# Kernel tuning notes

Hardware: AMD Instinct MI355X
Metric: run time of the kernel (lower is better)

## Reference

```python
import jax, jax.numpy as jnp
import numpy as np

GAMMA = 1.0  # rbf kernel bandwidth (config.gamma)
LN_EPS = 1e-5


def _layernorm(x, w):
    # LayerNorm(d_embed, bias=False): normalize last dim, scale by w
    mu = jnp.mean(x, axis=-1, keepdims=True)
    var = jnp.var(x, axis=-1, keepdims=True)
    return (x - mu) * jax.lax.rsqrt(var + LN_EPS) * w


def setup_inputs() -> dict:
    key = jax.random.key(0)
    ks = jax.random.split(key, 8)
    B, S, D, H = 4, 1024, 256, 8
    x = jax.random.normal(ks[0], (B, S, D), dtype=jnp.float32)
    e = jax.random.normal(ks[1], (B, S, D), dtype=jnp.float32)
    p = jax.random.normal(ks[2], (B, S, D), dtype=jnp.float32)
    W_q = 0.02 * jax.random.normal(ks[3], (H, D, D), dtype=jnp.float32)
    W_k = 0.02 * jax.random.normal(ks[4], (H, D, D), dtype=jnp.float32)
    W_v = 0.02 * jax.random.normal(ks[5], (H, D, D), dtype=jnp.float32)
    n_layer = 12
    W_o = (0.02 / np.sqrt(2 * n_layer)) * jax.random.normal(ks[6], (H * D, D), dtype=jnp.float32)
    ln_w = jnp.ones((D,), dtype=jnp.float32)
    return {"x": x, "e": e, "p": p, "W_q": W_q, "W_k": W_k, "W_v": W_v, "W_o": W_o, "ln_w": ln_w}


def reference(x, e, p, W_q, W_k, W_v, W_o, ln_w):
    # use_ppe=False path: only x is used (e, p ignored)
    B, S, D = x.shape
    H = W_q.shape[0]
    xn = _layernorm(x, ln_w)                                   # [B,S,D]
    # per-head full-size projections: Q/K/V [B,H,S,D]
    Q = jnp.einsum('bsd,hde->bhse', xn, W_q)
    K = jnp.einsum('bsd,hde->bhse', xn, W_k)
    V = jnp.einsum('bsd,hde->bhse', xn, W_v)
    # rbf kernel: exp(-gamma * ||q-k||^2) via the expansion trick
    q2 = jnp.sum(Q * Q, axis=-1)                               # [B,H,S]
    k2 = jnp.sum(K * K, axis=-1)                               # [B,H,S]
    qk = jnp.einsum('bhse,bhte->bhst', Q, K)                   # [B,H,S,S]
    dist2 = jnp.maximum(q2[..., :, None] + k2[..., None, :] - 2.0 * qk, 0.0)
    attn = jnp.exp(-GAMMA * dist2)                             # [B,H,S,S]
    # nto=True -> no causal mask; dropout=0 (eval) -> identity
    out = jnp.einsum('bhst,bhte->bhse', attn, V)               # [B,H,S,D]
    out = jnp.swapaxes(out, 1, 2).reshape(B, S, H * D)         # concat heads
    return out @ W_o                                           # [B,S,D]
```

## Files before the change

kernel.cpp:

```cpp
#include <hip/hip_runtime.h>
#include <cstdint>
#include <cstddef>

#define B_ 4
#define S_ 1024
#define D_ 256
#define H_ 8

typedef unsigned short u16;
typedef __attribute__((ext_vector_type(8))) short short8v;
typedef __attribute__((ext_vector_type(8))) _Float16 half8v;
typedef __attribute__((ext_vector_type(4))) float f32x4;
typedef __attribute__((ext_vector_type(4))) u16 u16x4;
typedef __attribute__((ext_vector_type(8))) u16 u16x8;

__device__ inline u16 f2b(float f) {
  unsigned u = __builtin_bit_cast(unsigned, f);
  unsigned r = (u + 0x7FFFu + ((u >> 16) & 1u)) >> 16;
  return (u16)r;
}
__device__ inline float b2f(u16 h) {
  return __builtin_bit_cast(float, ((unsigned)h) << 16);
}
__device__ inline u16 f2h(float f) {
  return __builtin_bit_cast(u16, (_Float16)f);
}
__device__ inline f32x4 mfma16(short8v a, short8v b, f32x4 c) {
  return __builtin_amdgcn_mfma_f32_16x16x32_bf16(a, b, c, 0, 0, 0);
}
__device__ inline f32x4 mfma16h(half8v a, half8v b, f32x4 c) {
  return __builtin_amdgcn_mfma_f32_16x16x32_f16(a, b, c, 0, 0, 0);
}
__device__ __forceinline__ void gl16(const u16* g, u16* l) {
  __builtin_amdgcn_global_load_lds((const uint32_t*)g, (uint32_t*)l, 16, 0, 0);
}

__global__ __launch_bounds__(256) void lnwt_kernel(
    const float* __restrict__ x, const float* __restrict__ w,
    const float* __restrict__ Wq, const float* __restrict__ Wk,
    const float* __restrict__ Wv, const float* __restrict__ Wo,
    u16* __restrict__ xf, u16* __restrict__ WTf, u16* __restrict__ WoTf) {
  const int bid = blockIdx.x;
  const int tid = threadIdx.x;
  if (bid < 4096) {
    const int row = bid;
    const float v = x[(size_t)row * D_ + tid];
    float s = v, s2 = v * v;
#pragma unroll
    for (int off = 32; off > 0; off >>= 1) {
      s  += __shfl_down(s, off);
      s2 += __shfl_down(s2, off);
    }
    __shared__ float rs[4], rs2[4];
    __shared__ float smu, srr;
    const int wid = tid >> 6, lane = tid & 63;
    if (lane == 0) { rs[wid] = s; rs2[wid] = s2; }
    __syncthreads();
    if (tid == 0) {
      const float a = rs[0] + rs[1] + rs[2] + rs[3];
      const float b = rs2[0] + rs2[1] + rs2[2] + rs2[3];
      const float mu  = a * (1.0f / D_);
      const float var = b * (1.0f / D_) - mu * mu;
      smu = mu; srr = rsqrtf(var + 1e-5f);
    }
    __syncthreads();
    const float r = (v - smu) * srr * w[tid];
    xf[(size_t)row * D_ + tid] = f2h(r);
  } else {
    __shared__ float t[32][33];
    const int z = bid - 4096;
    const int tc = tid & 31, tr = tid >> 5;
    if (z < 1536) {
      const int wm = z >> 6;
      const int mat = wm >> 3, h = wm & 7;
      const float* src = (mat == 0 ? Wq : mat == 1 ? Wk : Wv) + (size_t)h * 65536;
      const int t6 = z & 63;
      const int r0 = (t6 >> 3) * 32, c0 = (t6 & 7) * 32;
      u16* df = WTf + (size_t)wm * 65536;
#pragma unroll
      for (int i = 0; i < 4; ++i)
        t[tr + i * 8][tc] = src[(size_t)(r0 + tr + i * 8) * 256 + c0 + tc];
      __syncthreads();
#pragma unroll
      for (int i = 0; i < 4; ++i) {
        const float v = t[tc][tr + i * 8];
        df[(size_t)(c0 + tr + i * 8) * 256 + r0 + tc] = f2h(v);
      }
    } else {
      const int z2 = z - 1536;
      const int r0 = (z2 >> 3) * 32, c0 = (z2 & 7) * 32;
#pragma unroll
      for (int i = 0; i < 4; ++i)
        t[tr + i * 8][tc] = Wo[(size_t)(r0 + tr + i * 8) * 256 + c0 + tc];
      __syncthreads();
#pragma unroll
      for (int i = 0; i < 4; ++i) {
        const float v = t[tc][tr + i * 8];
        WoTf[(size_t)(c0 + tr + i * 8) * 2048 + r0 + tc] = f2b(v);
      }
    }
  }
}

__global__ __launch_bounds__(256, 3) void proj_kernel(
    const u16* __restrict__ xf, const u16* __restrict__ WTf,
    u16* __restrict__ Qf, u16* __restrict__ Kf,
    u16* __restrict__ Vt, float* __restrict__ k2g) {
  const int z = blockIdx.y;
  const int mat = z >> 3, h = z & 7;
  const int xb = blockIdx.x;

  const u16 *Ap, *Bp;
  int arow0, brow0;
  if (mat < 2) {
    Ap = WTf + (size_t)z * 65536; arow0 = (xb >> 5) * 128;
    Bp = xf;                      brow0 = (xb & 31) * 128;
  } else {
    Ap = xf;                      arow0 = (xb & 31) * 128;
    Bp = WTf + (size_t)z * 65536; brow0 = (xb >> 5) * 128;
  }

  __shared__ u16 LS[2 * 128 * 64];
  u16* AS = LS; u16* BS = LS + 128 * 64;
  char* LSb = (char*)LS;
  char* ASb = (char*)AS; char* BSb = (char*)BS;

  const int tid = threadIdx.x;
  const int w = tid >> 6, lane = tid & 63;
  const int lr = lane & 15, lh = lane >> 4;
  const int wm = w >> 1, wn = w & 1;

  f32x4 acc[4][4];
#pragma unroll
  for (int i = 0; i < 4; ++i)
#pragma unroll
    for (int j = 0; j < 4; ++j) acc[i][j] = (f32x4){0.f, 0.f, 0.f, 0.f};

  for (int k0 = 0; k0 < 256; k0 += 64) {
    __syncthreads();
#pragma unroll
    for (int j = 0; j < 4; ++j) {
      const int c0 = j * 256 + w * 64;
      const int c = c0 + lane;
      const int m = c >> 3, sl = c & 7;
      const int l = sl ^ (m & 7);
      gl16(Ap + (size_t)(arow0 + m) * 256 + k0 + l * 8, AS + c0 * 8);
    }
#pragma unroll
    for (int j = 0; j < 4; ++j) {
      const int c0 = j * 256 + w * 64;
      const int c = c0 + lane;
      const int n = c >> 3, sl = c & 7;
      const int l = sl ^ (n & 7);
      gl16(Bp + (size_t)(brow0 + n) * 256 + k0 + l * 8, BS + c0 * 8);
    }
    __syncthreads();

#pragma unroll
    for (int ks = 0; ks < 2; ++ks) {
      half8v af[4], bf[4];
#pragma unroll
      for (int mf = 0; mf < 4; ++mf) {
        const int m = wm * 64 + mf * 16 + lr;
        af[mf] = *reinterpret_cast<const half8v*>(
            ASb + m * 128 + (((ks * 4 + lh) * 16) ^ ((m & 7) << 4)));
      }
#pragma unroll
      for (int nf = 0; nf < 4; ++nf) {
        const int n = wn * 64 + nf * 16 + lr;
        bf[nf] = *reinterpret_cast<const half8v*>(
            BSb + n * 128 + (((ks * 4 + lh) * 16) ^ ((n & 7) << 4)));
      }
      __builtin_amdgcn_s_setprio(1);
#pragma unroll
      for (int mf = 0; mf < 4; ++mf)
#pragma unroll
        for (int nf = 0; nf < 4; ++nf)
          acc[mf][nf] = mfma16h(af[mf], bf[nf], acc[mf][nf]);
      __builtin_amdgcn_s_setprio(0);
    }
  }

  __syncthreads();

  if (mat < 2) {
    u16* Hf = (mat == 0) ? Qf : Kf;
#pragma unroll
    for (int mf = 0; mf < 4; ++mf)
#pragma unroll
      for (int nf = 0; nf < 4; ++nf) {
        const int sl_ = wn * 64 + nf * 16 + lr;
        const int el_ = wm * 64 + mf * 16 + lh * 4;
        u16x4 hv;
#pragma unroll
        for (int r = 0; r < 4; ++r) hv[r] = f2h(acc[mf][nf][r]);
        *reinterpret_cast<u16x4*>(LSb + sl_ * 256 + ((el_ * 2) ^ ((sl_ & 7) << 4))) = hv;
      }
    if (mat == 1) {
#pragma unroll
      for (int nf = 0; nf < 4; ++nf) {
        float p = 0.f;
#pragma unroll
        for (int mf = 0; mf < 4; ++mf)
#pragma unroll
          for (int r = 0; r < 4; ++r) {
            const float v = (float)(_Float16)acc[mf][nf][r];
            p = fmaf(v, v, p);
          }
        p += __shfl_xor(p, 16);
        p += __shfl_xor(p, 32);
        if (lh == 0) {
          const int s = brow0 + wn * 64 + nf * 16 + lr;
          const int bb = s >> 10;
          atomicAdd(&k2g[(size_t)(bb * H_ + h) * S_ + (s & 1023)], p);
        }
      }
    }
    __syncthreads();
#pragma unroll
    for (int i = 0; i < 8; ++i) {
      const int c = i * 256 + tid;
      const int sl_ = c >> 4, ch = c & 15;
      const u16x8 v = *reinterpret_cast<const u16x8*>(
          LSb + sl_ * 256 + ((ch * 16) ^ ((sl_ & 7) << 4)));
      const int s = brow0 + sl_;
      const int bb = s >> 10;
      *reinterpret_cast<u16x8*>(
          Hf + ((size_t)(bb * H_ + h) * S_ + (s & 1023)) * D_ + arow0 + ch * 8) = v;
    }
  } else {
#pragma unroll
    for (int mf = 0; mf < 4; ++mf)
#pragma unroll
      for (int nf = 0; nf < 4; ++nf) {
        const int dl_ = wn * 64 + nf * 16 + lr;
        const int sl_ = wm * 64 + mf * 16 + lh * 4;
        u16x4 hv;
#pragma unroll
        for (int r = 0; r < 4; ++r) hv[r] = f2b(acc[mf][nf][r]);
        *reinterpret_cast<u16x4*>(LSb + dl_ * 256 + ((sl_ * 2) ^ ((dl_ & 7) << 4))) = hv;
      }
    __syncthreads();
#pragma unroll
    for (int i = 0; i < 8; ++i) {
      const int c = i * 256 + tid;
      const int dl_ = c >> 4, ch = c & 15;
      const u16x8 v = *reinterpret_cast<const u16x8*>(
          LSb + dl_ * 256 + ((ch * 16) ^ ((dl_ & 7) << 4)));
      const int d = brow0 + dl_;
      const int sg = arow0 + ch * 8;
      const int bb = sg >> 10;
      *reinterpret_cast<u16x8*>(
          Vt + ((size_t)(bb * H_ + h) * D_ + d) * S_ + (sg & 1023)) = v;
    }
  }
}

__global__ __launch_bounds__(256, 2) void attn_kernel(
    const u16* __restrict__ Qf, const u16* __restrict__ Kf,
    const u16* __restrict__ Vt, const float* __restrict__ k2,
    u16* __restrict__ aOf) {
  const int bh  = blockIdx.x;
  const int qt  = blockIdx.y;
  const int tid = threadIdx.x;
  const int w = tid >> 6, lane = tid & 63;
  const int lr = lane & 15, lh = lane >> 4;
  const int qg = w >> 1, kvh = w & 1;

  __shared__ u16 KS[64 * 256];
  __shared__ u16 VS[256 * 64];
  __shared__ u16 PS[64 * 64];
  __shared__ float q2s[64];
  char* KB = (char*)KS; char* VB = (char*)VS; char* PB = (char*)PS;

  half8v qf[2][8];
#pragma unroll
  for (int at = 0; at < 2; ++at) {
    const int qrow = qt * 64 + qg * 32 + at * 16 + lr;
    const size_t qbase = ((size_t)(bh * S_) + qrow) * D_ + lh * 8;
#pragma unroll
    for (int ds = 0; ds < 8; ++ds)
      qf[at][ds] = *reinterpret_cast<const half8v*>(Qf + qbase + ds * 32);
  }
#pragma unroll
  for (int at = 0; at < 2; ++at) {
    float p = 0.f;
#pragma unroll
    for (int ds = 0; ds < 8; ++ds)
#pragma unroll
      for (int j = 0; j < 8; ++j) {
        const float v = (float)qf[at][ds][j];
        p = fmaf(v, v, p);
      }
    p += __shfl_xor(p, 16);
    p += __shfl_xor(p, 32);
    if (kvh == 0 && lh == 0) q2s[qg * 32 + at * 16 + lr] = p;
  }
  __syncthreads();
  float q2v[2][4];
#pragma unroll
  for (int at = 0; at < 2; ++at)
#pragma unroll
    for (int r = 0; r < 4; ++r)
      q2v[at][r] = q2s[qg * 32 + at * 16 + lh * 4 + r];

  f32x4 oacc[4][4];
#pragma unroll
  for (int i = 0; i < 4; ++i)
#pragma unroll
    for (int j = 0; j < 4; ++j) oacc[i][j] = (f32x4){0.f, 0.f, 0.f, 0.f};

  const size_t kgbase = (size_t)(bh * S_);
  const size_t vgbase = (size_t)(bh * D_);

  for (int kt = 0; kt < 16; ++kt) {
    __syncthreads();
#pragma unroll
    for (int j = 0; j < 8; ++j) {
      const int c0 = j * 256 + w * 64;
      const int c = c0 + lane;
      const int row = c >> 5, slot = c & 31;
      gl16(Kf + (kgbase + kt * 64 + row) * D_ + ((slot ^ (row & 7)) << 3), KS + c0 * 8);
    }
    __syncthreads();
#pragma unroll
    for (int j = 0; j < 8; ++j) {
      const int c0 = j * 256 + w * 64;
      const int c = c0 + lane;
      const int d = c >> 3, slot = c & 7;
      gl16(Vt + (vgbase + d) * S_ + kt * 64 + ((slot ^ (d & 7)) << 3), VS + c0 * 8);
    }

    f32x4 pacc[2][2];
#pragma unroll
    for (int at = 0; at < 2; ++at)
#pragma unroll
      for (int bt = 0; bt < 2; ++bt) pacc[at][bt] = (f32x4){0.f, 0.f, 0.f, 0.f};
#pragma unroll
    for (int ds = 0; ds < 8; ++ds) {
      half8v kf[2];
#pragma unroll
      for (int bt = 0; bt < 2; ++bt) {
        const int krow = kvh * 32 + bt * 16 + lr;
        kf[bt] = *reinterpret_cast<const half8v*>(
            KB + krow * 512 + (((ds * 64) + lh * 16) ^ ((krow & 7) << 4)));
      }
      __builtin_amdgcn_s_setprio(1);
#pragma unroll
      for (int at = 0; at < 2; ++at)
#pragma unroll
        for (int bt = 0; bt < 2; ++bt)
          pacc[at][bt] = mfma16h(qf[at][ds], kf[bt], pacc[at][bt]);
      __builtin_amdgcn_s_setprio(0);
    }
#pragma unroll
    for (int bt = 0; bt < 2; ++bt) {
      const int kv = kvh * 32 + bt * 16 + lr;
      const float k2v = k2[bh * S_ + kt * 64 + kv];
#pragma unroll
      for (int at = 0; at < 2; ++at)
#pragma unroll
        for (int r = 0; r < 4; ++r) {
          float d2 = q2v[at][r] + k2v - 2.0f * pacc[at][bt][r];
          d2 = fmaxf(d2, 0.f);
          const int q = qg * 32 + at * 16 + lh * 4 + r;
          *reinterpret_cast<u16*>(PB + q * 128 + ((kv * 2) ^ ((q & 7) << 4))) =
              f2b(__expf(-d2));
        }
    }
    __syncthreads();

    short8v vfr[4][2];
#pragma unroll
    for (int dt = 0; dt < 4; ++dt)
#pragma unroll
      for (int ks = 0; ks < 2; ++ks) {
        const int d = w * 64 + dt * 16 + lr;
        vfr[dt][ks] = *reinterpret_cast<const short8v*>(
            VB + d * 128 + (((ks * 64) + lh * 16) ^ ((d & 7) << 4)));
      }
#pragma unroll
    for (int pq = 0; pq < 4; ++pq) {
      short8v pa[2];
#pragma unroll
      for (int ks = 0; ks < 2; ++ks) {
        const int q = pq * 16 + lr;
        pa[ks] = *reinterpret_cast<const short8v*>(
            PB + q * 128 + (((ks * 64) + lh * 16) ^ ((q & 7) << 4)));
      }
      __builtin_amdgcn_s_setprio(1);
#pragma unroll
      for (int dt = 0; dt < 4; ++dt) {
        oacc[pq][dt] = mfma16(pa[0], vfr[dt][0], oacc[pq][dt]);
        oacc[pq][dt] = mfma16(pa[1], vfr[dt][1], oacc[pq][dt]);
      }
      __builtin_amdgcn_s_setprio(0);
    }
  }

  const int bb = bh >> 3, hh = bh & 7;
#pragma unroll
  for (int pq = 0; pq < 4; ++pq)
#pragma unroll
    for (int dt = 0; dt < 4; ++dt)
#pragma unroll
      for (int r = 0; r < 4; ++r) {
        const int s = qt * 64 + pq * 16 + lh * 4 + r;
        const int d = w * 64 + dt * 16 + lr;
        const size_t idx = ((size_t)(bb * S_) + s) * (H_ * D_) + hh * D_ + d;
        aOf[idx] = f2b(oacc[pq][dt][r]);
      }
}

__global__ __launch_bounds__(512, 4) void outproj_kernel(
    const u16* __restrict__ WoTf, const u16* __restrict__ aOf,
    u16* __restrict__ pbuf) {
  const int xb = blockIdx.x;
  const int kc = blockIdx.y;
  const int bm = xb >> 5, bn = xb & 31;
  const int arow0 = bm * 128, brow0 = bn * 128;

  __shared__ u16 AhS[128 * 64], BhS[128 * 64];
  char* AhB = (char*)AhS; char* BhB = (char*)BhS;

  const int tid = threadIdx.x;
  const int w = tid >> 6, lane = tid & 63;
  const int lr = lane & 15, lh = lane >> 4;
  const int wr = w >> 2, wc = w & 3;

  f32x4 acc[4][2];
#pragma unroll
  for (int i = 0; i < 4; ++i)
#pragma unroll
    for (int j = 0; j < 2; ++j) acc[i][j] = (f32x4){0.f, 0.f, 0.f, 0.f};

  for (int k0 = kc * 512; k0 < kc * 512 + 512; k0 += 64) {
#pragma unroll
    for (int i = 0; i < 2; ++i) {
      const int c = tid + i * 512;
      const int row = c >> 3, slot = c & 7;
      const int off = row * 128 + ((slot * 16) ^ ((row & 7) << 4));
      const size_t ga = (size_t)(arow0 + row) * 2048 + k0 + slot * 8;
      const size_t gb = (size_t)(brow0 + row) * 2048 + k0 + slot * 8;
      *reinterpret_cast<short8v*>(AhB + off) = *reinterpret_cast<const short8v*>(WoTf + ga);
      *reinterpret_cast<short8v*>(BhB + off) = *reinterpret_cast<const short8v*>(aOf + gb);
    }
    __syncthreads();
#pragma unroll
    for (int ks = 0; ks < 2; ++ks) {
      short8v afh[4], bfh[2];
#pragma unroll
      for (int mf = 0; mf < 4; ++mf) {
        const int m = wr * 64 + mf * 16 + lr;
        afh[mf] = *reinterpret_cast<const short8v*>(
            AhB + m * 128 + (((ks * 64) + lh * 16) ^ ((m & 7) << 4)));
      }
#pragma unroll
      for (int nf = 0; nf < 2; ++nf) {
        const int n = wc * 32 + nf * 16 + lr;
        bfh[nf] = *reinterpret_cast<const short8v*>(
            BhB + n * 128 + (((ks * 64) + lh * 16) ^ ((n & 7) << 4)));
      }
      __builtin_amdgcn_s_setprio(1);
#pragma unroll
      for (int mf = 0; mf < 4; ++mf)
#pragma unroll
        for (int nf = 0; nf < 2; ++nf)
          acc[mf][nf] = mfma16(afh[mf], bfh[nf], acc[mf][nf]);
      __builtin_amdgcn_s_setprio(0);
    }
    __syncthreads();
  }

  u16* pout = pbuf + (size_t)kc * (4096 * 256);
#pragma unroll
  for (int mf = 0; mf < 4; ++mf) {
    const int e0 = bm * 128 + wr * 64 + mf * 16 + lh * 4;
#pragma unroll
    for (int nf = 0; nf < 2; ++nf) {
      const int s = bn * 128 + wc * 32 + nf * 16 + lr;
      u16x4 hv;
#pragma unroll
      for (int r = 0; r < 4; ++r) hv[r] = f2b(acc[mf][nf][r]);
      *reinterpret_cast<u16x4*>(pout + (size_t)s * D_ + e0) = hv;
    }
  }
}

__global__ __launch_bounds__(256) void reduce_kernel(const u16* __restrict__ pbuf,
                                                     float* __restrict__ out) {
  const size_t i = ((size_t)blockIdx.x * 256 + threadIdx.x) * 8;
  const size_t C = (size_t)4096 * 256;
  const u16x8 a = *reinterpret_cast<const u16x8*>(pbuf + i);
  const u16x8 b = *reinterpret_cast<const u16x8*>(pbuf + C + i);
  const u16x8 c = *reinterpret_cast<const u16x8*>(pbuf + 2 * C + i);
  const u16x8 d = *reinterpret_cast<const u16x8*>(pbuf + 3 * C + i);
  float4 o0, o1;
  float* o = &o0.x;
#pragma unroll
  for (int j = 0; j < 8; ++j) {
    const float v = b2f((u16)a[j]) + b2f((u16)b[j]) + b2f((u16)c[j]) + b2f((u16)d[j]);
    if (j < 4) (&o0.x)[j] = v; else (&o1.x)[j - 4] = v;
  }
  (void)o;
  *reinterpret_cast<float4*>(out + i)     = o0;
  *reinterpret_cast<float4*>(out + i + 4) = o1;
}

extern "C" void kernel_launch(void* const* d_in, const int* in_sizes, int n_in,
                              void* d_out, int out_size, void* d_ws, size_t ws_size,
                              hipStream_t stream) {
  (void)in_sizes; (void)n_in; (void)out_size; (void)ws_size;
  const float* x   = (const float*)d_in[0];
  const float* Wq  = (const float*)d_in[3];
  const float* Wk  = (const float*)d_in[4];
  const float* Wv  = (const float*)d_in[5];
  const float* Wo  = (const float*)d_in[6];
  const float* lnw = (const float*)d_in[7];
  float* out = (float*)d_out;

  char* ws = (char*)d_ws;
  u16*  xf   = (u16*)(ws);
  u16*  WTf  = (u16*)(ws + ((size_t)2   << 20));
  u16*  WoTf = (u16*)(ws + ((size_t)5   << 20));
  float* k2  = (float*)(ws + ((size_t)6  << 20));
  u16*  Qf   = (u16*)(ws + ((size_t)8   << 20));
  u16*  Kf   = (u16*)(ws + ((size_t)24  << 20));
  u16*  Vt   = (u16*)(ws + ((size_t)40  << 20));
  u16*  aOf  = (u16*)(ws + ((size_t)56  << 20));
  u16*  pbuf = (u16*)(ws + ((size_t)72  << 20));

  hipMemsetAsync(k2, 0, (size_t)B_ * H_ * S_ * sizeof(float), stream);
  lnwt_kernel<<<dim3(6144), dim3(256), 0, stream>>>(x, lnw, Wq, Wk, Wv, Wo, xf, WTf, WoTf);
  proj_kernel<<<dim3(64, 24), dim3(256), 0, stream>>>(xf, WTf, Qf, Kf, Vt, k2);
  attn_kernel<<<dim3(32, 16), dim3(256), 0, stream>>>(Qf, Kf, Vt, k2, aOf);
  outproj_kernel<<<dim3(64, 4), dim3(512), 0, stream>>>(WoTf, aOf, pbuf);
  reduce_kernel<<<dim3(512), dim3(256), 0, stream>>>(pbuf, out);
}
```

Before: 98.53 us.

## Prefetch next K/V tile during compute and drop q2 shared-memory exchange

Restructures the attention kernel's main loop so the next K tile is loaded right after QK^T finishes and the next V tile right after PV finishes, using explicit vmcnt waits and raw barriers instead of __syncthreads. The QK MFMA operands are swapped so each lane keeps its own q2 row in a register, which removes the shared-memory q2 buffer and one barrier, and lets P be written as packed 4-element stores with vectorised k2 loads. The goal is to hide global-to-LDS latency behind MFMA work and cut synchronisation and scattered LDS writes. The hand-written waitcnt counts and the wraparound prefetch on the last iteration rely on exact ordering of outstanding loads, so any miscount would cause a race.

```diff
diff --git a/kernel.cpp b/kernel.cpp
--- a/kernel.cpp
+++ b/kernel.cpp
@@ -270,7 +270,6 @@
   __shared__ u16 KS[64 * 256];
   __shared__ u16 VS[256 * 64];
   __shared__ u16 PS[64 * 64];
-  __shared__ float q2s[64];
   char* KB = (char*)KS; char* VB = (char*)VS; char* PB = (char*)PS;
 
   half8v qf[2][8];
@@ -282,6 +281,26 @@
     for (int ds = 0; ds < 8; ++ds)
       qf[at][ds] = *reinterpret_cast<const half8v*>(Qf + qbase + ds * 32);
   }
+
+  const size_t kgbase = (size_t)(bh * S_);
+  const size_t vgbase = (size_t)(bh * D_);
+
+#pragma unroll
+  for (int j = 0; j < 8; ++j) {
+    const int c0 = j * 256 + w * 64;
+    const int c = c0 + lane;
+    const int row = c >> 5, slot = c & 31;
+    gl16(Kf + (kgbase + row) * D_ + ((slot ^ (row & 7)) << 3), KS + c0 * 8);
+  }
+#pragma unroll
+  for (int j = 0; j < 8; ++j) {
+    const int c0 = j * 256 + w * 64;
+    const int c = c0 + lane;
+    const int d = c >> 3, slot = c & 7;
+    gl16(Vt + (vgbase + d) * S_ + ((slot ^ (d & 7)) << 3), VS + c0 * 8);
+  }
+
+  float q2v[2];
 #pragma unroll
   for (int at = 0; at < 2; ++at) {
     float p = 0.f;
@@ -294,15 +313,12 @@
       }
     p += __shfl_xor(p, 16);
     p += __shfl_xor(p, 32);
-    if (kvh == 0 && lh == 0) q2s[qg * 32 + at * 16 + lr] = p;
-  }
-  __syncthreads();
-  float q2v[2][4];
-#pragma unroll
-  for (int at = 0; at < 2; ++at)
-#pragma unroll
-    for (int r = 0; r < 4; ++r)
-      q2v[at][r] = q2s[qg * 32 + at * 16 + lh * 4 + r];
+    q2v[at] = p;
+  }
+
+  asm volatile("s_waitcnt vmcnt(8)" ::: "memory");
+  __builtin_amdgcn_sched_barrier(0);
+  __builtin_amdgcn_s_barrier();
 
   f32x4 oacc[4][4];
 #pragma unroll
@@ -310,93 +326,109 @@
 #pragma unroll
     for (int j = 0; j < 4; ++j) oacc[i][j] = (f32x4){0.f, 0.f, 0.f, 0.f};
 
-  const size_t kgbase = (size_t)(bh * S_);
-  const size_t vgbase = (size_t)(bh * D_);
-
   for (int kt = 0; kt < 16; ++kt) {
-    __syncthreads();
+    const int ktn = (kt + 1) & 15;
+
+    f32x4 k2v[2];
+#pragma unroll
+    for (int bt = 0; bt < 2; ++bt)
+      k2v[bt] = *reinterpret_cast<const f32x4*>(
+          k2 + (size_t)bh * S_ + kt * 64 + kvh * 32 + bt * 16 + lh * 4);
+
+    f32x4 pacc[2][2];
+#pragma unroll
+    for (int at = 0; at < 2; ++at)
+#pragma unroll
+      for (int bt = 0; bt < 2; ++bt) pacc[at][bt] = (f32x4){0.f, 0.f, 0.f, 0.f};
+#pragma unroll
+    for (int ds = 0; ds < 8; ++ds) {
+      half8v kf[2];
+#pragma unroll
+      for (int bt = 0; bt < 2; ++bt) {
+        const int krow = kvh * 32 + bt * 16 + lr;
+        kf[bt] = *reinterpret_cast<const half8v*>(
+            KB + krow * 512 + (((ds * 64) + lh * 16) ^ ((krow & 7) << 4)));
+      }
+      __builtin_amdgcn_s_setprio(1);
+#pragma unroll
+      for (int at = 0; at < 2; ++at)
+#pragma unroll
+        for (int bt = 0; bt < 2; ++bt)
+          pacc[at][bt] = mfma16h(kf[bt], qf[at][ds], pacc[at][bt]);
+      __builtin_amdgcn_s_setprio(0);
+    }
+    asm volatile("s_waitcnt lgkmcnt(0)" ::: "memory");
+    __builtin_amdgcn_sched_barrier(0);
+    __builtin_amdgcn_s_barrier();
+
 #pragma unroll
     for (int j = 0; j < 8; ++j) {
       const int c0 = j * 256 + w * 64;
       const int c = c0 + lane;
       const int row = c >> 5, slot = c & 31;
-      gl16(Kf + (kgbase + kt * 64 + row) * D_ + ((slot ^ (row & 7)) << 3), KS + c0 * 8);
-    }
-    __syncthreads();
+      gl16(Kf + (kgbase + ktn * 64 + row) * D_ + ((slot ^ (row & 7)) << 3), KS + c0 * 8);
+    }
+
+#pragma unroll
+    for (int at = 0; at < 2; ++at) {
+      const int q = qg * 32 + at * 16 + lr;
+#pragma unroll
+      for (int bt = 0; bt < 2; ++bt) {
+        const int kv0 = kvh * 32 + bt * 16 + lh * 4;
+        u16x4 pv;
+#pragma unroll
+        for (int r = 0; r < 4; ++r) {
+          float d2 = q2v[at] + k2v[bt][r] - 2.0f * pacc[at][bt][r];
+          d2 = fmaxf(d2, 0.f);
+          pv[r] = f2b(__expf(-d2));
+        }
+        *reinterpret_cast<u16x4*>(PB + q * 128 + ((kv0 * 2) ^ ((q & 7) << 4))) = pv;
+      }
+    }
+    asm volatile("s_waitcnt vmcnt(8) lgkmcnt(0)" ::: "memory");
+    __builtin_amdgcn_sched_barrier(0);
+    __builtin_amdgcn_s_barrier();
+
+    short8v vfr[4][2];
+#pragma unroll
+    for (int dt = 0; dt < 4; ++dt)
+#pragma unroll
+      for (int ks = 0; ks < 2; ++ks) {
+        const int d = w * 64 + dt * 16 + lr;
+        vfr[dt][ks] = *reinterpret_cast<const short8v*>(
+            VB + d * 128 + (((ks * 64) + lh * 16) ^ ((d & 7) << 4)));
+      }
+#pragma unroll
+    for (int pq = 0; pq < 4; ++pq) {
+      short8v pa[2];
+#pragma unroll
+      for (int ks = 0; ks < 2; ++ks) {
+        const int q = pq * 16 + lr;
+        pa[ks] = *reinterpret_cast<const short8v*>(
+            PB + q * 128 + (((ks * 64) + lh * 16) ^ ((q & 7) << 4)));
+      }
+      __builtin_amdgcn_s_setprio(1);
+#pragma unroll
+      for (int dt = 0; dt < 4; ++dt) {
+        oacc[pq][dt] = mfma16(pa[0], vfr[dt][0], oacc[pq][dt]);
+        oacc[pq][dt] = mfma16(pa[1], vfr[dt][1], oacc[pq][dt]);
+      }
+      __builtin_amdgcn_s_setprio(0);
+    }
+    asm volatile("s_waitcnt vmcnt(0) lgkmcnt(0)" ::: "memory");
+    __builtin_amdgcn_sched_barrier(0);
+    __builtin_amdgcn_s_barrier();
+
 #pragma unroll
     for (int j = 0; j < 8; ++j) {
       const int c0 = j * 256 + w * 64;
       const int c = c0 + lane;
       const int d = c >> 3, slot = c & 7;
-      gl16(Vt + (vgbase + d) * S_ + kt * 64 + ((slot ^ (d & 7)) << 3), VS + c0 * 8);
-    }
-
-    f32x4 pacc[2][2];
-#pragma unroll
-    for (int at = 0; at < 2; ++at)
-#pragma unroll
-      for (int bt = 0; bt < 2; ++bt) pacc[at][bt] = (f32x4){0.f, 0.f, 0.f, 0.f};
-#pragma unroll
-    for (int ds = 0; ds < 8; ++ds) {
-      half8v kf[2];
-#pragma unroll
-      for (int bt = 0; bt < 2; ++bt) {
-        const int krow = kvh * 32 + bt * 16 + lr;
-        kf[bt] = *reinterpret_cast<const half8v*>(
-            KB + krow * 512 + (((ds * 64) + lh * 16) ^ ((krow & 7) << 4)));
-      }
-      __builtin_amdgcn_s_setprio(1);
-#pragma unroll
-      for (int at = 0; at < 2; ++at)
-#pragma unroll
-        for (int bt = 0; bt < 2; ++bt)
-          pacc[at][bt] = mfma16h(qf[at][ds], kf[bt], pacc[at][bt]);
-      __builtin_amdgcn_s_setprio(0);
-    }
-#pragma unroll
-    for (int bt = 0; bt < 2; ++bt) {
-      const int kv = kvh * 32 + bt * 16 + lr;
-      const float k2v = k2[bh * S_ + kt * 64 + kv];
-#pragma unroll
-      for (int at = 0; at < 2; ++at)
-#pragma unroll
-        for (int r = 0; r < 4; ++r) {
-          float d2 = q2v[at][r] + k2v - 2.0f * pacc[at][bt][r];
-          d2 = fmaxf(d2, 0.f);
-          const int q = qg * 32 + at * 16 + lh * 4 + r;
-          *reinterpret_cast<u16*>(PB + q * 128 + ((kv * 2) ^ ((q & 7) << 4))) =
-              f2b(__expf(-d2));
-        }
-    }
-    __syncthreads();
-
-    short8v vfr[4][2];
-#pragma unroll
-    for (int dt = 0; dt < 4; ++dt)
-#pragma unroll
-      for (int ks = 0; ks < 2; ++ks) {
-        const int d = w * 64 + dt * 16 + lr;
-        vfr[dt][ks] = *reinterpret_cast<const short8v*>(
-            VB + d * 128 + (((ks * 64) + lh * 16) ^ ((d & 7) << 4)));
-      }
-#pragma unroll
-    for (int pq = 0; pq < 4; ++pq) {
-      short8v pa[2];
-#pragma unroll
-      for (int ks = 0; ks < 2; ++ks) {
-        const int q = pq * 16 + lr;
-        pa[ks] = *reinterpret_cast<const short8v*>(
-            PB + q * 128 + (((ks * 64) + lh * 16) ^ ((q & 7) << 4)));
-      }
-      __builtin_amdgcn_s_setprio(1);
-#pragma unroll
-      for (int dt = 0; dt < 4; ++dt) {
-        oacc[pq][dt] = mfma16(pa[0], vfr[dt][0], oacc[pq][dt]);
-        oacc[pq][dt] = mfma16(pa[1], vfr[dt][1], oacc[pq][dt]);
-      }
-      __builtin_amdgcn_s_setprio(0);
-    }
-  }
+      gl16(Vt + (vgbase + d) * S_ + ktn * 64 + ((slot ^ (d & 7)) << 3), VS + c0 * 8);
+    }
+  }
+
+  asm volatile("s_waitcnt vmcnt(0)" ::: "memory");
 
   const int bb = bh >> 3, hh = bh & 7;
 #pragma unroll
```

New measurement: 97.74 us. About the same (-0.8%).

## Load K/V fragments directly from global into registers, double-buffer P tile

Applied to the files above, without the earlier changes.

The attention kernel stops staging K and V tiles through shared memory. Each wave loads its K and V MFMA fragments straight from global memory into registers, and the QK MFMA is transposed (K as the A operand) so that q2 and k2 can be taken per lane without a shared-memory exchange. The P tile is double-buffered so only one barrier per iteration remains, which cuts LDS traffic, LDS footprint and synchronisation. The cost is redundant global/L2 reads, since both wave pairs and all q-tiles reload the same K/V, plus higher register pressure.

```diff
diff --git a/kernel.cpp b/kernel.cpp
--- a/kernel.cpp
+++ b/kernel.cpp
@@ -267,11 +267,8 @@
   const int lr = lane & 15, lh = lane >> 4;
   const int qg = w >> 1, kvh = w & 1;
 
-  __shared__ u16 KS[64 * 256];
-  __shared__ u16 VS[256 * 64];
-  __shared__ u16 PS[64 * 64];
-  __shared__ float q2s[64];
-  char* KB = (char*)KS; char* VB = (char*)VS; char* PB = (char*)PS;
+  __shared__ u16 PS[2][64 * 64];
+  char* PB = (char*)PS;
 
   half8v qf[2][8];
 #pragma unroll
@@ -282,6 +279,8 @@
     for (int ds = 0; ds < 8; ++ds)
       qf[at][ds] = *reinterpret_cast<const half8v*>(Qf + qbase + ds * 32);
   }
+
+  float q2v[2];
 #pragma unroll
   for (int at = 0; at < 2; ++at) {
     float p = 0.f;
@@ -294,15 +293,13 @@
       }
     p += __shfl_xor(p, 16);
     p += __shfl_xor(p, 32);
-    if (kvh == 0 && lh == 0) q2s[qg * 32 + at * 16 + lr] = p;
-  }
-  __syncthreads();
-  float q2v[2][4];
-#pragma unroll
-  for (int at = 0; at < 2; ++at)
-#pragma unroll
-    for (int r = 0; r < 4; ++r)
-      q2v[at][r] = q2s[qg * 32 + at * 16 + lh * 4 + r];
+    q2v[at] = p;
+  }
+
+  const u16* kp0 = Kf + ((size_t)bh * S_ + kvh * 32 + lr) * D_ + lh * 8;
+  const u16* kp1 = kp0 + 16 * D_;
+  const u16* vp  = Vt + ((size_t)bh * D_ + w * 64 + lr) * S_ + lh * 8;
+  const float* k2p = k2 + (size_t)bh * S_ + kvh * 32 + lh * 4;
 
   f32x4 oacc[4][4];
 #pragma unroll
@@ -310,26 +307,20 @@
 #pragma unroll
     for (int j = 0; j < 4; ++j) oacc[i][j] = (f32x4){0.f, 0.f, 0.f, 0.f};
 
-  const size_t kgbase = (size_t)(bh * S_);
-  const size_t vgbase = (size_t)(bh * D_);
-
   for (int kt = 0; kt < 16; ++kt) {
-    __syncthreads();
-#pragma unroll
-    for (int j = 0; j < 8; ++j) {
-      const int c0 = j * 256 + w * 64;
-      const int c = c0 + lane;
-      const int row = c >> 5, slot = c & 31;
-      gl16(Kf + (kgbase + kt * 64 + row) * D_ + ((slot ^ (row & 7)) << 3), KS + c0 * 8);
-    }
-    __syncthreads();
-#pragma unroll
-    for (int j = 0; j < 8; ++j) {
-      const int c0 = j * 256 + w * 64;
-      const int c = c0 + lane;
-      const int d = c >> 3, slot = c & 7;
-      gl16(Vt + (vgbase + d) * S_ + kt * 64 + ((slot ^ (d & 7)) << 3), VS + c0 * 8);
-    }
+    half8v kfA0[4], kfA1[4], kfB0[4], kfB1[4];
+#pragma unroll
+    for (int ds = 0; ds < 4; ++ds) {
+      kfA0[ds] = *reinterpret_cast<const half8v*>(kp0 + ds * 32);
+      kfA1[ds] = *reinterpret_cast<const half8v*>(kp1 + ds * 32);
+    }
+#pragma unroll
+    for (int ds = 0; ds < 4; ++ds) {
+      kfB0[ds] = *reinterpret_cast<const half8v*>(kp0 + 128 + ds * 32);
+      kfB1[ds] = *reinterpret_cast<const half8v*>(kp1 + 128 + ds * 32);
+    }
+    const f32x4 k2v0 = *reinterpret_cast<const f32x4*>(k2p);
+    const f32x4 k2v1 = *reinterpret_cast<const f32x4*>(k2p + 16);
 
     f32x4 pacc[2][2];
 #pragma unroll
@@ -337,65 +328,71 @@
 #pragma unroll
       for (int bt = 0; bt < 2; ++bt) pacc[at][bt] = (f32x4){0.f, 0.f, 0.f, 0.f};
 #pragma unroll
-    for (int ds = 0; ds < 8; ++ds) {
-      half8v kf[2];
+    for (int ds = 0; ds < 4; ++ds) {
+      __builtin_amdgcn_s_setprio(1);
+      pacc[0][0] = mfma16h(kfA0[ds], qf[0][ds], pacc[0][0]);
+      pacc[0][1] = mfma16h(kfA1[ds], qf[0][ds], pacc[0][1]);
+      pacc[1][0] = mfma16h(kfA0[ds], qf[1][ds], pacc[1][0]);
+      pacc[1][1] = mfma16h(kfA1[ds], qf[1][ds], pacc[1][1]);
+      __builtin_amdgcn_s_setprio(0);
+    }
+
+    short8v vf[4][2];
+#pragma unroll
+    for (int dt = 0; dt < 4; ++dt)
+#pragma unroll
+      for (int ks = 0; ks < 2; ++ks)
+        vf[dt][ks] = *reinterpret_cast<const short8v*>(vp + dt * 16 * S_ + ks * 32);
+
+#pragma unroll
+    for (int ds = 0; ds < 4; ++ds) {
+      __builtin_amdgcn_s_setprio(1);
+      pacc[0][0] = mfma16h(kfB0[ds], qf[0][ds + 4], pacc[0][0]);
+      pacc[0][1] = mfma16h(kfB1[ds], qf[0][ds + 4], pacc[0][1]);
+      pacc[1][0] = mfma16h(kfB0[ds], qf[1][ds + 4], pacc[1][0]);
+      pacc[1][1] = mfma16h(kfB1[ds], qf[1][ds + 4], pacc[1][1]);
+      __builtin_amdgcn_s_setprio(0);
+    }
+
+    char* psw = PB + ((kt & 1) << 13);
+#pragma unroll
+    for (int at = 0; at < 2; ++at) {
+      const int q = qg * 32 + at * 16 + lr;
 #pragma unroll
       for (int bt = 0; bt < 2; ++bt) {
-        const int krow = kvh * 32 + bt * 16 + lr;
-        kf[bt] = *reinterpret_cast<const half8v*>(
-            KB + krow * 512 + (((ds * 64) + lh * 16) ^ ((krow & 7) << 4)));
-      }
+        const f32x4 k2v = bt ? k2v1 : k2v0;
+        const int kv0 = kvh * 32 + bt * 16 + lh * 4;
+        u16x4 pv;
+#pragma unroll
+        for (int r = 0; r < 4; ++r) {
+          float d2 = q2v[at] + k2v[r] - 2.0f * pacc[at][bt][r];
+          d2 = fmaxf(d2, 0.f);
+          pv[r] = f2b(__expf(-d2));
+        }
+        *reinterpret_cast<u16x4*>(psw + q * 128 + ((kv0 * 2) ^ ((q & 7) << 4))) = pv;
+      }
+    }
+    asm volatile("s_waitcnt lgkmcnt(0)" ::: "memory");
+    __builtin_amdgcn_sched_barrier(0);
+    __builtin_amdgcn_s_barrier();
+
+#pragma unroll
+    for (int pq = 0; pq < 4; ++pq) {
+      const int q = pq * 16 + lr;
+      const short8v pa0 = *reinterpret_cast<const short8v*>(
+          psw + q * 128 + ((lh * 16) ^ ((q & 7) << 4)));
+      const short8v pa1 = *reinterpret_cast<const short8v*>(
+          psw + q * 128 + ((64 + lh * 16) ^ ((q & 7) << 4)));
       __builtin_amdgcn_s_setprio(1);
 #pragma unroll
-      for (int at = 0; at < 2; ++at)
-#pragma unroll
-        for (int bt = 0; bt < 2; ++bt)
-          pacc[at][bt] = mfma16h(qf[at][ds], kf[bt], pacc[at][bt]);
+      for (int dt = 0; dt < 4; ++dt) {
+        oacc[pq][dt] = mfma16(pa0, vf[dt][0], oacc[pq][dt]);
+        oacc[pq][dt] = mfma16(pa1, vf[dt][1], oacc[pq][dt]);
+      }
       __builtin_amdgcn_s_setprio(0);
     }
-#pragma unroll
-    for (int bt = 0; bt < 2; ++bt) {
-      const int kv = kvh * 32 + bt * 16 + lr;
-      const float k2v = k2[bh * S_ + kt * 64 + kv];
-#pragma unroll
-      for (int at = 0; at < 2; ++at)
-#pragma unroll
-        for (int r = 0; r < 4; ++r) {
-          float d2 = q2v[at][r] + k2v - 2.0f * pacc[at][bt][r];
-          d2 = fmaxf(d2, 0.f);
-          const int q = qg * 32 + at * 16 + lh * 4 + r;
-          *reinterpret_cast<u16*>(PB + q * 128 + ((kv * 2) ^ ((q & 7) << 4))) =
-              f2b(__expf(-d2));
-        }
-    }
-    __syncthreads();
-
-    short8v vfr[4][2];
-#pragma unroll
-    for (int dt = 0; dt < 4; ++dt)
-#pragma unroll
-      for (int ks = 0; ks < 2; ++ks) {
-        const int d = w * 64 + dt * 16 + lr;
-        vfr[dt][ks] = *reinterpret_cast<const short8v*>(
-            VB + d * 128 + (((ks * 64) + lh * 16) ^ ((d & 7) << 4)));
-      }
-#pragma unroll
-    for (int pq = 0; pq < 4; ++pq) {
-      short8v pa[2];
-#pragma unroll
-      for (int ks = 0; ks < 2; ++ks) {
-        const int q = pq * 16 + lr;
-        pa[ks] = *reinterpret_cast<const short8v*>(
-            PB + q * 128 + (((ks * 64) + lh * 16) ^ ((q & 7) << 4)));
-      }
-      __builtin_amdgcn_s_setprio(1);
-#pragma unroll
-      for (int dt = 0; dt < 4; ++dt) {
-        oacc[pq][dt] = mfma16(pa[0], vfr[dt][0], oacc[pq][dt]);
-        oacc[pq][dt] = mfma16(pa[1], vfr[dt][1], oacc[pq][dt]);
-      }
-      __builtin_amdgcn_s_setprio(0);
-    }
+
+    kp0 += 64 * D_; kp1 += 64 * D_; vp += 64; k2p += 64;
   }
 
   const int bb = bh >> 3, hh = bh & 7;
```

After: 142.1 us. 1.44x slower.
